# Kernel optimization log

Measured on AMD Instinct MI355X. Metric: run time of the kernel, lower is better.

The kernel has to match this reference:

```python
import jax, jax.numpy as jnp
import numpy as np

N = 100000   # nodes
E = 1600000  # edges
IN, HID, OUT = 128, 256, 64


def _glorot(key, shape):
    fan_in, fan_out = shape[1], shape[0]
    lim = (6.0 / (fan_in + fan_out)) ** 0.5
    return jax.random.uniform(key, shape, jnp.float32, -lim, lim)


def setup_inputs() -> dict:
    key = jax.random.key(0)
    ks = jax.random.split(key, 8)
    x = jax.random.normal(ks[0], (N, IN), jnp.float32)
    edge_index = jax.random.randint(ks[1], (2, E), 0, N, jnp.int64)
    # SAGEConv params: lin_l (neighbor path, has bias), lin_r (root path, no bias)
    return {
        "x": x,
        "edge_index": edge_index,
        "W1_l": _glorot(ks[2], (HID, IN)),
        "b1": jnp.zeros((HID,), jnp.float32),
        "W1_r": _glorot(ks[3], (HID, IN)),
        "W2_l": _glorot(ks[4], (OUT, HID)),
        "b2": jnp.zeros((OUT,), jnp.float32),
        "W2_r": _glorot(ks[5], (OUT, HID)),
    }


def _sage_conv(x, src, dst, W_l, b, W_r):
    # mean aggregation of neighbor features at destination nodes
    msg = x[src]                                             # [E, d] gather
    agg = jax.ops.segment_sum(msg, dst, num_segments=N)      # [N, d]
    cnt = jax.ops.segment_sum(jnp.ones((src.shape[0],), jnp.float32), dst,
                              num_segments=N)                # [N]
    mean = agg / jnp.maximum(cnt, 1.0)[:, None]
    return mean @ W_l.T + b + x @ W_r.T


def reference(x, edge_index, W1_l, b1, W1_r, W2_l, b2, W2_r):
    src, dst = edge_index[0], edge_index[1]
    h = jax.nn.relu(_sage_conv(x, src, dst, W1_l, b1, W1_r))
    # dropout is identity in eval mode
    return _sage_conv(h, src, dst, W2_l, b2, W2_r)
```

## Files before the change

kernel.cpp:

```cpp
#include <hip/hip_runtime.h>
#include <hip/hip_bf16.h>

#define NNODE 100000
#define NEDGE 1600000
#define NBBLK 512
#define CHUNK (NEDGE / NBBLK)
#define NB2 ((NNODE + 1023) >> 10)

typedef __attribute__((ext_vector_type(8))) short bf16x8;
typedef __attribute__((ext_vector_type(4))) float f32x4;
typedef __attribute__((ext_vector_type(2))) float f32x2;

__device__ __forceinline__ unsigned short f2bf(float f){
  unsigned u = __float_as_uint(f);
  u += 0x7fffu + ((u >> 16) & 1u);
  return (unsigned short)(u >> 16);
}
__device__ __forceinline__ unsigned pk2(float a, float b){
  return (unsigned)f2bf(a) | ((unsigned)f2bf(b) << 16);
}
__device__ __forceinline__ float bflo(unsigned v){ return __uint_as_float(v << 16); }
__device__ __forceinline__ float bfhi(unsigned v){ return __uint_as_float(v & 0xffff0000u); }

__global__ __launch_bounds__(256) void k_xh(const float* __restrict__ x,
                                            unsigned* __restrict__ A1u,
                                            unsigned* __restrict__ x8u,
                                            const int* __restrict__ dst,
                                            unsigned* __restrict__ gh){
  int bid = blockIdx.x;
  if (bid < NBBLK){
    __shared__ unsigned h[NB2];
    for (int t = threadIdx.x; t < NB2; t += 256) h[t] = 0;
    __syncthreads();
    int base = bid * CHUNK;
    for (int j = threadIdx.x; j < CHUNK; j += 256)
      atomicAdd(&h[dst[base + j] >> 10], 1u);
    __syncthreads();
    for (int t = threadIdx.x; t < NB2; t += 256) gh[bid * NB2 + t] = h[t];
    return;
  }
  int i = (bid - NBBLK) * 256 + threadIdx.x;
  if (i >= NNODE * 32) return;
  float4 v = ((const float4*)x)[i];
  int e = i * 4;
  int row = e >> 7, c = e & 127;
  unsigned* d = A1u + (size_t)row * 128 + 64 + (c >> 1);
  d[0] = pk2(v.x, v.y);
  d[1] = pk2(v.z, v.w);
  unsigned p = (unsigned)__builtin_amdgcn_cvt_pk_fp8_f32(v.x, v.y, 0, false);
  p = (unsigned)__builtin_amdgcn_cvt_pk_fp8_f32(v.z, v.w, (int)p, true);
  x8u[(size_t)row * 32 + (c >> 2)] = p;
}

__global__ __launch_bounds__(512) void k_scan512(const unsigned* __restrict__ gh,
                                                 unsigned* __restrict__ gbase,
                                                 unsigned* __restrict__ btot){
  int b = blockIdx.x, t = threadIdx.x;
  int lane = t & 63, wv = t >> 6;
  unsigned v = gh[t * NB2 + b];
  unsigned s = v;
  #pragma unroll
  for (int off = 1; off < 64; off <<= 1){
    unsigned u = __shfl_up(s, off, 64);
    if (lane >= off) s += u;
  }
  __shared__ unsigned wsum[8];
  if (lane == 63) wsum[wv] = s;
  __syncthreads();
  unsigned woff = 0;
  for (int w = 0; w < wv; ++w) woff += wsum[w];
  gbase[t * NB2 + b] = woff + s - v;
  if (t == 511) btot[b] = woff + s;
}

__global__ __launch_bounds__(128) void k_scanb(const unsigned* __restrict__ btot,
                                               unsigned* __restrict__ bbase,
                                               unsigned* __restrict__ rowptr){
  __shared__ unsigned buf[128];
  int tid = threadIdx.x;
  unsigned v = (tid < NB2) ? btot[tid] : 0u;
  buf[tid] = v;
  __syncthreads();
  #pragma unroll
  for (int off = 1; off < 128; off <<= 1){
    unsigned t = (tid >= off) ? buf[tid - off] : 0u;
    __syncthreads();
    buf[tid] += t;
    __syncthreads();
  }
  if (tid < NB2) bbase[tid] = buf[tid] - v;
  if (tid == 0){ bbase[NB2] = NEDGE; rowptr[NNODE] = NEDGE; }
}

__global__ __launch_bounds__(256) void k_binscat(const int* __restrict__ src,
                                                 const int* __restrict__ dst,
                                                 const unsigned* __restrict__ gbase,
                                                 const unsigned* __restrict__ bbase,
                                                 unsigned* __restrict__ pairs){
  __shared__ unsigned cur[NB2];
  for (int t = threadIdx.x; t < NB2; t += 256)
    cur[t] = bbase[t] + gbase[blockIdx.x * NB2 + t];
  __syncthreads();
  int base = blockIdx.x * CHUNK;
  for (int j = threadIdx.x; j < CHUNK; j += 256){
    int s = src[base + j], d = dst[base + j];
    unsigned p = atomicAdd(&cur[d >> 10], 1u);
    pairs[p] = ((unsigned)s << 10) | (unsigned)(d & 1023);
  }
}

__global__ __launch_bounds__(1024) void k_buildcsr(const unsigned* __restrict__ bbase,
                                                   const unsigned* __restrict__ pairs,
                                                   unsigned* __restrict__ rowptr,
                                                   unsigned* __restrict__ col){
  __shared__ unsigned hist[1024];
  __shared__ unsigned wsum[16];
  const int b = blockIdx.x, tid = threadIdx.x;
  const int lane = tid & 63, wv = tid >> 6;
  const unsigned e0 = bbase[b], e1 = bbase[b + 1];
  const int nb0 = b << 10;
  hist[tid] = 0;
  __syncthreads();
  for (unsigned j = e0 + tid; j < e1; j += 1024)
    atomicAdd(&hist[pairs[j] & 1023u], 1u);
  __syncthreads();
  unsigned v = hist[tid];
  unsigned s = v;
  #pragma unroll
  for (int off = 1; off < 64; off <<= 1){
    unsigned u = __shfl_up(s, off, 64);
    if (lane >= off) s += u;
  }
  if (lane == 63) wsum[wv] = s;
  __syncthreads();
  unsigned woff = 0;
  for (int w = 0; w < wv; ++w) woff += wsum[w];
  unsigned gpos = e0 + woff + s - v;
  if (nb0 + tid < NNODE) rowptr[nb0 + tid] = gpos;
  __syncthreads();
  hist[tid] = gpos;
  __syncthreads();
  for (unsigned j = e0 + tid; j < e1; j += 1024){
    unsigned e = pairs[j];
    unsigned p = atomicAdd(&hist[e & 1023u], 1u);
    col[p] = e >> 10;
  }
}

__global__ void k_wcvt(const float* __restrict__ W1l, const float* __restrict__ W1r,
                       const float* __restrict__ W2l, const float* __restrict__ W2r,
                       unsigned short* __restrict__ Bwt1, unsigned short* __restrict__ Bwt2){
  int i = blockIdx.x * 256 + threadIdx.x;
  if (i < 256 * 256){
    int n = i >> 8, k = i & 255;
    float v = (k < 128) ? W1l[n * 128 + k] : W1r[n * 128 + (k - 128)];
    Bwt1[i] = f2bf(v);
  }
  int i2 = i - 256 * 256;
  if (i2 >= 0 && i2 < 128 * 256){
    int n = i2 >> 8, k = i2 & 255;
    float v = (n < 64) ? W2l[n * 256 + k] : W2r[(n - 64) * 256 + k];
    Bwt2[i2] = f2bf(v);
  }
}

__global__ __launch_bounds__(256) void k_agg1(const unsigned* __restrict__ rowptr,
                                              const unsigned* __restrict__ col,
                                              const unsigned* __restrict__ x8u,
                                              unsigned* __restrict__ A1u){
  int gw = (blockIdx.x * 256 + threadIdx.x) >> 6;
  int lane = threadIdx.x & 63;
  if (gw >= NNODE) return;
  unsigned s0 = rowptr[gw], s1 = rowptr[gw + 1];
  const int sel = lane >> 4, u = lane & 15;
  const uint2* x82 = (const uint2*)x8u;
  float a0=0.f,a1=0.f,a2=0.f,a3=0.f,a4=0.f,a5=0.f,a6=0.f,a7=0.f;
  f32x2 p;
  unsigned j = s0;
  for (; j + 15 < s1; j += 16){
    unsigned ca = col[j + sel], cb = col[j + 4 + sel];
    unsigned cc = col[j + 8 + sel], cd = col[j + 12 + sel];
    uint2 va = x82[(size_t)ca * 16 + u];
    uint2 vb = x82[(size_t)cb * 16 + u];
    uint2 vc = x82[(size_t)cc * 16 + u];
    uint2 vd = x82[(size_t)cd * 16 + u];
    p = __builtin_amdgcn_cvt_pk_f32_fp8((int)va.x, false); a0+=p.x; a1+=p.y;
    p = __builtin_amdgcn_cvt_pk_f32_fp8((int)va.x, true ); a2+=p.x; a3+=p.y;
    p = __builtin_amdgcn_cvt_pk_f32_fp8((int)va.y, false); a4+=p.x; a5+=p.y;
    p = __builtin_amdgcn_cvt_pk_f32_fp8((int)va.y, true ); a6+=p.x; a7+=p.y;
    p = __builtin_amdgcn_cvt_pk_f32_fp8((int)vb.x, false); a0+=p.x; a1+=p.y;
    p = __builtin_amdgcn_cvt_pk_f32_fp8((int)vb.x, true ); a2+=p.x; a3+=p.y;
    p = __builtin_amdgcn_cvt_pk_f32_fp8((int)vb.y, false); a4+=p.x; a5+=p.y;
    p = __builtin_amdgcn_cvt_pk_f32_fp8((int)vb.y, true ); a6+=p.x; a7+=p.y;
    p = __builtin_amdgcn_cvt_pk_f32_fp8((int)vc.x, false); a0+=p.x; a1+=p.y;
    p = __builtin_amdgcn_cvt_pk_f32_fp8((int)vc.x, true ); a2+=p.x; a3+=p.y;
    p = __builtin_amdgcn_cvt_pk_f32_fp8((int)vc.y, false); a4+=p.x; a5+=p.y;
    p = __builtin_amdgcn_cvt_pk_f32_fp8((int)vc.y, true ); a6+=p.x; a7+=p.y;
    p = __builtin_amdgcn_cvt_pk_f32_fp8((int)vd.x, false); a0+=p.x; a1+=p.y;
    p = __builtin_amdgcn_cvt_pk_f32_fp8((int)vd.x, true ); a2+=p.x; a3+=p.y;
    p = __builtin_amdgcn_cvt_pk_f32_fp8((int)vd.y, false); a4+=p.x; a5+=p.y;
    p = __builtin_amdgcn_cvt_pk_f32_fp8((int)vd.y, true ); a6+=p.x; a7+=p.y;
  }
  for (; j + 3 < s1; j += 4){
    unsigned ca = col[j + sel];
    uint2 va = x82[(size_t)ca * 16 + u];
    p = __builtin_amdgcn_cvt_pk_f32_fp8((int)va.x, false); a0+=p.x; a1+=p.y;
    p = __builtin_amdgcn_cvt_pk_f32_fp8((int)va.x, true ); a2+=p.x; a3+=p.y;
    p = __builtin_amdgcn_cvt_pk_f32_fp8((int)va.y, false); a4+=p.x; a5+=p.y;
    p = __builtin_amdgcn_cvt_pk_f32_fp8((int)va.y, true ); a6+=p.x; a7+=p.y;
  }
  int rem = (int)(s1 - j);
  if (sel < rem){
    unsigned ca = col[j + sel];
    uint2 va = x82[(size_t)ca * 16 + u];
    p = __builtin_amdgcn_cvt_pk_f32_fp8((int)va.x, false); a0+=p.x; a1+=p.y;
    p = __builtin_amdgcn_cvt_pk_f32_fp8((int)va.x, true ); a2+=p.x; a3+=p.y;
    p = __builtin_amdgcn_cvt_pk_f32_fp8((int)va.y, false); a4+=p.x; a5+=p.y;
    p = __builtin_amdgcn_cvt_pk_f32_fp8((int)va.y, true ); a6+=p.x; a7+=p.y;
  }
  a0 += __shfl_xor(a0, 16, 64); a1 += __shfl_xor(a1, 16, 64);
  a2 += __shfl_xor(a2, 16, 64); a3 += __shfl_xor(a3, 16, 64);
  a4 += __shfl_xor(a4, 16, 64); a5 += __shfl_xor(a5, 16, 64);
  a6 += __shfl_xor(a6, 16, 64); a7 += __shfl_xor(a7, 16, 64);
  a0 += __shfl_xor(a0, 32, 64); a1 += __shfl_xor(a1, 32, 64);
  a2 += __shfl_xor(a2, 32, 64); a3 += __shfl_xor(a3, 32, 64);
  a4 += __shfl_xor(a4, 32, 64); a5 += __shfl_xor(a5, 32, 64);
  a6 += __shfl_xor(a6, 32, 64); a7 += __shfl_xor(a7, 32, 64);
  if (lane < 16){
    float inv = 1.f / fmaxf((float)(s1 - s0), 1.f);
    uint4 w;
    w.x = pk2(a0 * inv, a1 * inv);
    w.y = pk2(a2 * inv, a3 * inv);
    w.z = pk2(a4 * inv, a5 * inv);
    w.w = pk2(a6 * inv, a7 * inv);
    *(uint4*)(A1u + (size_t)gw * 128 + 4 * lane) = w;
  }
}

template<int BN, bool RELU, bool BIAS, int MODE>
__global__ __launch_bounds__(256) void k_gemm(const unsigned short* __restrict__ A,
                                              const unsigned short* __restrict__ B,
                                              const float* __restrict__ bias,
                                              unsigned short* __restrict__ C,
                                              unsigned char* __restrict__ z8,
                                              unsigned short* __restrict__ r16,
                                              int nrows){
  constexpr int NF = BN / 64;
  __shared__ unsigned short a_t[64 * 64];
  __shared__ unsigned short b_t[BN * 64];
  const int tid = threadIdx.x, wave = tid >> 6, lane = tid & 63;
  const int row0 = blockIdx.x * 64;
  char* ab = (char*)a_t;
  char* bb = (char*)b_t;

  f32x4 acc[4][NF];
  #pragma unroll
  for (int m = 0; m < 4; ++m)
    #pragma unroll
    for (int n = 0; n < NF; ++n)
      acc[m][n] = (f32x4){0.f, 0.f, 0.f, 0.f};

  for (int kt = 0; kt < 4; ++kt){
    {
      int r = tid >> 2;
      int gr = row0 + r; if (gr > nrows - 1) gr = nrows - 1;
      const uint4* s4 = (const uint4*)(A + (size_t)gr * 256 + kt * 64);
      int c0 = (tid & 3) * 2;
      uint4 v0 = s4[c0], v1 = s4[c0 + 1];
      *(uint4*)(ab + r * 128 + ((c0 * 16) ^ ((r & 7) << 4))) = v0;
      *(uint4*)(ab + r * 128 + (((c0 + 1) * 16) ^ ((r & 7) << 4))) = v1;
    }
    {
      constexpr int CPT = BN / 32;
      #pragma unroll
      for (int c = 0; c < CPT; ++c){
        int gc = tid * CPT + c;
        int n = gc >> 3, ck = gc & 7;
        uint4 v = ((const uint4*)(B + (size_t)n * 256 + kt * 64))[ck];
        *(uint4*)(bb + n * 128 + ((ck * 16) ^ ((n & 7) << 4))) = v;
      }
    }
    __syncthreads();
    #pragma unroll
    for (int kk = 0; kk < 2; ++kk){
      int k2 = (kk * 32 + ((lane >> 4) * 8)) * 2;
      bf16x8 af[4];
      #pragma unroll
      for (int m = 0; m < 4; ++m){
        int rr = m * 16 + (lane & 15);
        af[m] = *(const bf16x8*)(ab + rr * 128 + (k2 ^ ((rr & 7) << 4)));
      }
      #pragma unroll
      for (int n = 0; n < NF; ++n){
        int cc = wave * (16 * NF) + n * 16 + (lane & 15);
        bf16x8 bfv = *(const bf16x8*)(bb + cc * 128 + (k2 ^ ((cc & 7) << 4)));
        #pragma unroll
        for (int m = 0; m < 4; ++m)
          acc[m][n] = __builtin_amdgcn_mfma_f32_16x16x32_bf16(af[m], bfv, acc[m][n], 0, 0, 0);
      }
    }
    __syncthreads();
  }
  #pragma unroll
  for (int m = 0; m < 4; ++m){
    int rbase = row0 + m * 16 + ((lane >> 4) << 2);
    #pragma unroll
    for (int r = 0; r < 4; ++r){
      if (rbase + r < nrows){
        #pragma unroll
        for (int n = 0; n < NF; ++n){
          int cc = wave * (16 * NF) + n * 16 + (lane & 15);
          float v = acc[m][n][r];
          if (BIAS) v += bias[cc];
          if (RELU) v = fmaxf(v, 0.f);
          if (MODE == 0){
            C[(size_t)(rbase + r) * BN + cc] = f2bf(v);
          } else {
            if (cc < 64)
              z8[(size_t)(rbase + r) * 64 + cc] =
                (unsigned char)__builtin_amdgcn_cvt_pk_fp8_f32(v, v, 0, false);
            else
              r16[(size_t)(rbase + r) * 64 + (cc - 64)] = f2bf(v);
          }
        }
      }
    }
  }
}

__global__ __launch_bounds__(256) void k_agg2(const unsigned* __restrict__ rowptr,
                                              const unsigned* __restrict__ col,
                                              const unsigned* __restrict__ z8u,
                                              const unsigned* __restrict__ r16u,
                                              const float* __restrict__ b2,
                                              float* __restrict__ out){
  int gw = (blockIdx.x * 256 + threadIdx.x) >> 6;
  int lane = threadIdx.x & 63;
  if (gw >= NNODE) return;
  unsigned s0 = rowptr[gw], s1 = rowptr[gw + 1];
  const int sel = lane >> 4, u = lane & 15;
  float a0=0.f,a1=0.f,a2=0.f,a3=0.f;
  f32x2 p;
  unsigned j = s0;
  for (; j + 15 < s1; j += 16){
    unsigned ca = col[j + sel], cb = col[j + 4 + sel];
    unsigned cc = col[j + 8 + sel], cd = col[j + 12 + sel];
    unsigned va = z8u[(size_t)ca * 16 + u];
    unsigned vb = z8u[(size_t)cb * 16 + u];
    unsigned vc = z8u[(size_t)cc * 16 + u];
    unsigned vd = z8u[(size_t)cd * 16 + u];
    p = __builtin_amdgcn_cvt_pk_f32_fp8((int)va, false); a0+=p.x; a1+=p.y;
    p = __builtin_amdgcn_cvt_pk_f32_fp8((int)va, true ); a2+=p.x; a3+=p.y;
    p = __builtin_amdgcn_cvt_pk_f32_fp8((int)vb, false); a0+=p.x; a1+=p.y;
    p = __builtin_amdgcn_cvt_pk_f32_fp8((int)vb, true ); a2+=p.x; a3+=p.y;
    p = __builtin_amdgcn_cvt_pk_f32_fp8((int)vc, false); a0+=p.x; a1+=p.y;
    p = __builtin_amdgcn_cvt_pk_f32_fp8((int)vc, true ); a2+=p.x; a3+=p.y;
    p = __builtin_amdgcn_cvt_pk_f32_fp8((int)vd, false); a0+=p.x; a1+=p.y;
    p = __builtin_amdgcn_cvt_pk_f32_fp8((int)vd, true ); a2+=p.x; a3+=p.y;
  }
  for (; j + 3 < s1; j += 4){
    unsigned ca = col[j + sel];
    unsigned va = z8u[(size_t)ca * 16 + u];
    p = __builtin_amdgcn_cvt_pk_f32_fp8((int)va, false); a0+=p.x; a1+=p.y;
    p = __builtin_amdgcn_cvt_pk_f32_fp8((int)va, true ); a2+=p.x; a3+=p.y;
  }
  int rem = (int)(s1 - j);
  if (sel < rem){
    unsigned ca = col[j + sel];
    unsigned va = z8u[(size_t)ca * 16 + u];
    p = __builtin_amdgcn_cvt_pk_f32_fp8((int)va, false); a0+=p.x; a1+=p.y;
    p = __builtin_amdgcn_cvt_pk_f32_fp8((int)va, true ); a2+=p.x; a3+=p.y;
  }
  a0 += __shfl_xor(a0, 16, 64); a1 += __shfl_xor(a1, 16, 64);
  a2 += __shfl_xor(a2, 16, 64); a3 += __shfl_xor(a3, 16, 64);
  a0 += __shfl_xor(a0, 32, 64); a1 += __shfl_xor(a1, 32, 64);
  a2 += __shfl_xor(a2, 32, 64); a3 += __shfl_xor(a3, 32, 64);
  if (lane < 16){
    float inv = 1.f / fmaxf((float)(s1 - s0), 1.f);
    uint2 rv = ((const uint2*)(r16u + (size_t)gw * 32))[lane];
    float4 bv = ((const float4*)b2)[lane];
    float4 res;
    res.x = a0 * inv + bflo(rv.x) + bv.x;
    res.y = a1 * inv + bfhi(rv.x) + bv.y;
    res.z = a2 * inv + bflo(rv.y) + bv.z;
    res.w = a3 * inv + bfhi(rv.y) + bv.w;
    ((float4*)out)[(size_t)gw * 16 + lane] = res;
  }
}

extern "C" void kernel_launch(void* const* d_in, const int* in_sizes, int n_in,
                              void* d_out, int out_size, void* d_ws, size_t ws_size,
                              hipStream_t stream) {
  const float* x   = (const float*)d_in[0];
  const int*   ei  = (const int*)d_in[1];
  const float* W1l = (const float*)d_in[2];
  const float* b1  = (const float*)d_in[3];
  const float* W1r = (const float*)d_in[4];
  const float* W2l = (const float*)d_in[5];
  const float* b2  = (const float*)d_in[6];
  const float* W2r = (const float*)d_in[7];
  float* out = (float*)d_out;

  char* ws = (char*)d_ws;
  size_t off = 0;
  auto alloc = [&](size_t bytes) -> void* {
    void* p = ws + off;
    off = (off + bytes + 255) & ~(size_t)255;
    return p;
  };
  unsigned* rowptr = (unsigned*)alloc((size_t)(NNODE + 1) * 4);
  unsigned* col    = (unsigned*)alloc((size_t)NEDGE * 4);
  unsigned* pairs  = (unsigned*)alloc((size_t)NEDGE * 4);
  unsigned* gh     = (unsigned*)alloc((size_t)NBBLK * NB2 * 4);
  unsigned* gbase  = (unsigned*)alloc((size_t)NBBLK * NB2 * 4);
  unsigned* btot   = (unsigned*)alloc((size_t)NB2 * 4);
  unsigned* bbase  = (unsigned*)alloc((size_t)(NB2 + 1) * 4);
  unsigned short* A1   = (unsigned short*)alloc((size_t)NNODE * 256 * 2);
  unsigned short* h    = (unsigned short*)alloc((size_t)NNODE * 256 * 2);
  unsigned short* r16  = (unsigned short*)alloc((size_t)NNODE * 64 * 2);
  unsigned* x8u        = (unsigned*)alloc((size_t)NNODE * 32 * 4);
  unsigned char* z8    = (unsigned char*)alloc((size_t)NNODE * 64);
  unsigned short* Bwt1 = (unsigned short*)alloc(256 * 256 * 2);
  unsigned short* Bwt2 = (unsigned short*)alloc(128 * 256 * 2);

  const int* srcv = ei;
  const int* dstv = ei + NEDGE;

  k_xh<<<NBBLK + (NNODE * 32 + 255) / 256, 256, 0, stream>>>(x, (unsigned*)A1, x8u, dstv, gh);
  k_scan512<<<NB2, 512, 0, stream>>>(gh, gbase, btot);
  k_scanb<<<1, 128, 0, stream>>>(btot, bbase, rowptr);
  k_binscat<<<NBBLK, 256, 0, stream>>>(srcv, dstv, gbase, bbase, pairs);
  k_buildcsr<<<NB2, 1024, 0, stream>>>(bbase, pairs, rowptr, col);

  k_wcvt<<<(256 * 256 + 128 * 256 + 255) / 256, 256, 0, stream>>>(W1l, W1r, W2l, W2r, Bwt1, Bwt2);

  k_agg1<<<(NNODE + 3) / 4, 256, 0, stream>>>(rowptr, col, x8u, (unsigned*)A1);

  int gblocks = (NNODE + 63) / 64;
  k_gemm<256, true,  true,  0><<<gblocks, 256, 0, stream>>>(A1, Bwt1, b1, h, nullptr, nullptr, NNODE);
  k_gemm<128, false, false, 2><<<gblocks, 256, 0, stream>>>(h,  Bwt2, nullptr, nullptr, z8, r16, NNODE);

  k_agg2<<<(NNODE + 3) / 4, 256, 0, stream>>>(rowptr, col, (const unsigned*)z8, (const unsigned*)r16, b2, out);
}
```

Before: 314.2 us.

## Fold scans and weight conversion into fewer kernels; use finer buckets and 128-row GEMM tiles

The CSR build now uses 512-node buckets instead of 1024-node buckets, which gives 196 buckets. The separate bucket-base scan kernel is removed, and each binscat and buildcsr block recomputes that scan redundantly in shared memory. The weight bf16 conversion is merged into the first x-conversion/histogram kernel, so two launches are dropped. The GEMM kernels move to 512-thread blocks covering 128 rows, with waves split 2x4 so each staged B tile is reused across more rows. The cost is redundant scan work in every block and more shared memory per GEMM block, which may lower occupancy.

```diff
diff --git a/kernel.cpp b/kernel.cpp
--- a/kernel.cpp
+++ b/kernel.cpp
@@ -5,7 +5,9 @@
 #define NEDGE 1600000
 #define NBBLK 512
 #define CHUNK (NEDGE / NBBLK)
-#define NB2 ((NNODE + 1023) >> 10)
+#define NBUCK ((NNODE + 511) >> 9)
+#define XB ((NNODE * 32 + 255) / 256)
+#define WB 384
 
 typedef __attribute__((ext_vector_type(8))) short bf16x8;
 typedef __attribute__((ext_vector_type(4))) float f32x4;
@@ -26,30 +28,50 @@
                                             unsigned* __restrict__ A1u,
                                             unsigned* __restrict__ x8u,
                                             const int* __restrict__ dst,
-                                            unsigned* __restrict__ gh){
+                                            unsigned* __restrict__ gh,
+                                            const float* __restrict__ W1l,
+                                            const float* __restrict__ W1r,
+                                            const float* __restrict__ W2l,
+                                            const float* __restrict__ W2r,
+                                            unsigned short* __restrict__ Bwt1,
+                                            unsigned short* __restrict__ Bwt2){
   int bid = blockIdx.x;
   if (bid < NBBLK){
-    __shared__ unsigned h[NB2];
-    for (int t = threadIdx.x; t < NB2; t += 256) h[t] = 0;
+    __shared__ unsigned h[NBUCK];
+    for (int t = threadIdx.x; t < NBUCK; t += 256) h[t] = 0;
     __syncthreads();
     int base = bid * CHUNK;
     for (int j = threadIdx.x; j < CHUNK; j += 256)
-      atomicAdd(&h[dst[base + j] >> 10], 1u);
-    __syncthreads();
-    for (int t = threadIdx.x; t < NB2; t += 256) gh[bid * NB2 + t] = h[t];
+      atomicAdd(&h[dst[base + j] >> 9], 1u);
+    __syncthreads();
+    for (int t = threadIdx.x; t < NBUCK; t += 256) gh[bid * NBUCK + t] = h[t];
     return;
   }
-  int i = (bid - NBBLK) * 256 + threadIdx.x;
-  if (i >= NNODE * 32) return;
-  float4 v = ((const float4*)x)[i];
-  int e = i * 4;
-  int row = e >> 7, c = e & 127;
-  unsigned* d = A1u + (size_t)row * 128 + 64 + (c >> 1);
-  d[0] = pk2(v.x, v.y);
-  d[1] = pk2(v.z, v.w);
-  unsigned p = (unsigned)__builtin_amdgcn_cvt_pk_fp8_f32(v.x, v.y, 0, false);
-  p = (unsigned)__builtin_amdgcn_cvt_pk_fp8_f32(v.z, v.w, (int)p, true);
-  x8u[(size_t)row * 32 + (c >> 2)] = p;
+  if (bid < NBBLK + XB){
+    int i = (bid - NBBLK) * 256 + threadIdx.x;
+    if (i >= NNODE * 32) return;
+    float4 v = ((const float4*)x)[i];
+    int e = i * 4;
+    int row = e >> 7, c = e & 127;
+    unsigned* d = A1u + (size_t)row * 128 + 64 + (c >> 1);
+    d[0] = pk2(v.x, v.y);
+    d[1] = pk2(v.z, v.w);
+    unsigned p = (unsigned)__builtin_amdgcn_cvt_pk_fp8_f32(v.x, v.y, 0, false);
+    p = (unsigned)__builtin_amdgcn_cvt_pk_fp8_f32(v.z, v.w, (int)p, true);
+    x8u[(size_t)row * 32 + (c >> 2)] = p;
+    return;
+  }
+  int i = (bid - NBBLK - XB) * 256 + threadIdx.x;
+  if (i < 256 * 256){
+    int n = i >> 8, k = i & 255;
+    float v = (k < 128) ? W1l[n * 128 + k] : W1r[n * 128 + (k - 128)];
+    Bwt1[i] = f2bf(v);
+  } else if (i < 256 * 256 + 128 * 256){
+    int i2 = i - 256 * 256;
+    int n = i2 >> 8, k = i2 & 255;
+    float v = (n < 64) ? W2l[n * 256 + k] : W2r[(n - 64) * 256 + k];
+    Bwt2[i2] = f2bf(v);
+  }
 }
 
 __global__ __launch_bounds__(512) void k_scan512(const unsigned* __restrict__ gh,
@@ -57,7 +79,7 @@
                                                  unsigned* __restrict__ btot){
   int b = blockIdx.x, t = threadIdx.x;
   int lane = t & 63, wv = t >> 6;
-  unsigned v = gh[t * NB2 + b];
+  unsigned v = gh[t * NBUCK + b];
   unsigned s = v;
   #pragma unroll
   for (int off = 1; off < 64; off <<= 1){
@@ -69,60 +91,72 @@
   __syncthreads();
   unsigned woff = 0;
   for (int w = 0; w < wv; ++w) woff += wsum[w];
-  gbase[t * NB2 + b] = woff + s - v;
+  gbase[t * NBUCK + b] = woff + s - v;
   if (t == 511) btot[b] = woff + s;
-}
-
-__global__ __launch_bounds__(128) void k_scanb(const unsigned* __restrict__ btot,
-                                               unsigned* __restrict__ bbase,
-                                               unsigned* __restrict__ rowptr){
-  __shared__ unsigned buf[128];
-  int tid = threadIdx.x;
-  unsigned v = (tid < NB2) ? btot[tid] : 0u;
-  buf[tid] = v;
-  __syncthreads();
-  #pragma unroll
-  for (int off = 1; off < 128; off <<= 1){
-    unsigned t = (tid >= off) ? buf[tid - off] : 0u;
-    __syncthreads();
-    buf[tid] += t;
-    __syncthreads();
-  }
-  if (tid < NB2) bbase[tid] = buf[tid] - v;
-  if (tid == 0){ bbase[NB2] = NEDGE; rowptr[NNODE] = NEDGE; }
 }
 
 __global__ __launch_bounds__(256) void k_binscat(const int* __restrict__ src,
                                                  const int* __restrict__ dst,
                                                  const unsigned* __restrict__ gbase,
-                                                 const unsigned* __restrict__ bbase,
+                                                 const unsigned* __restrict__ btot,
                                                  unsigned* __restrict__ pairs){
-  __shared__ unsigned cur[NB2];
-  for (int t = threadIdx.x; t < NB2; t += 256)
-    cur[t] = bbase[t] + gbase[blockIdx.x * NB2 + t];
+  __shared__ unsigned sb[256];
+  __shared__ unsigned cur[NBUCK];
+  int t = threadIdx.x;
+  unsigned v = (t < NBUCK) ? btot[t] : 0u;
+  sb[t] = v;
+  __syncthreads();
+  #pragma unroll
+  for (int off = 1; off < 256; off <<= 1){
+    unsigned u = (t >= off) ? sb[t - off] : 0u;
+    __syncthreads();
+    sb[t] += u;
+    __syncthreads();
+  }
+  if (t < NBUCK) cur[t] = (sb[t] - v) + gbase[blockIdx.x * NBUCK + t];
   __syncthreads();
   int base = blockIdx.x * CHUNK;
-  for (int j = threadIdx.x; j < CHUNK; j += 256){
+  for (int j = t; j < CHUNK; j += 256){
     int s = src[base + j], d = dst[base + j];
-    unsigned p = atomicAdd(&cur[d >> 10], 1u);
-    pairs[p] = ((unsigned)s << 10) | (unsigned)(d & 1023);
-  }
-}
-
-__global__ __launch_bounds__(1024) void k_buildcsr(const unsigned* __restrict__ bbase,
-                                                   const unsigned* __restrict__ pairs,
-                                                   unsigned* __restrict__ rowptr,
-                                                   unsigned* __restrict__ col){
-  __shared__ unsigned hist[1024];
-  __shared__ unsigned wsum[16];
+    unsigned p = atomicAdd(&cur[d >> 9], 1u);
+    pairs[p] = ((unsigned)s << 9) | (unsigned)(d & 511);
+  }
+}
+
+__global__ __launch_bounds__(512) void k_buildcsr(const unsigned* __restrict__ btot,
+                                                  const unsigned* __restrict__ pairs,
+                                                  unsigned* __restrict__ rowptr,
+                                                  unsigned* __restrict__ col){
+  __shared__ unsigned sb[256];
+  __shared__ unsigned hist[512];
+  __shared__ unsigned wsum[8];
+  __shared__ unsigned se0, se1;
   const int b = blockIdx.x, tid = threadIdx.x;
   const int lane = tid & 63, wv = tid >> 6;
-  const unsigned e0 = bbase[b], e1 = bbase[b + 1];
-  const int nb0 = b << 10;
+  if (tid < 256){
+    unsigned v = (tid < NBUCK) ? btot[tid] : 0u;
+    sb[tid] = v;
+  }
+  __syncthreads();
+  #pragma unroll
+  for (int off = 1; off < 256; off <<= 1){
+    unsigned u = 0;
+    if (tid < 256 && tid >= off) u = sb[tid - off];
+    __syncthreads();
+    if (tid < 256) sb[tid] += u;
+    __syncthreads();
+  }
+  if (tid == 0){
+    se1 = sb[b];
+    se0 = sb[b] - btot[b];
+    if (b == 0) rowptr[NNODE] = NEDGE;
+  }
   hist[tid] = 0;
   __syncthreads();
-  for (unsigned j = e0 + tid; j < e1; j += 1024)
-    atomicAdd(&hist[pairs[j] & 1023u], 1u);
+  const unsigned e0 = se0, e1 = se1;
+  const int nb0 = b << 9;
+  for (unsigned j = e0 + tid; j < e1; j += 512)
+    atomicAdd(&hist[pairs[j] & 511u], 1u);
   __syncthreads();
   unsigned v = hist[tid];
   unsigned s = v;
@@ -140,27 +174,10 @@
   __syncthreads();
   hist[tid] = gpos;
   __syncthreads();
-  for (unsigned j = e0 + tid; j < e1; j += 1024){
+  for (unsigned j = e0 + tid; j < e1; j += 512){
     unsigned e = pairs[j];
-    unsigned p = atomicAdd(&hist[e & 1023u], 1u);
-    col[p] = e >> 10;
-  }
-}
-
-__global__ void k_wcvt(const float* __restrict__ W1l, const float* __restrict__ W1r,
-                       const float* __restrict__ W2l, const float* __restrict__ W2r,
-                       unsigned short* __restrict__ Bwt1, unsigned short* __restrict__ Bwt2){
-  int i = blockIdx.x * 256 + threadIdx.x;
-  if (i < 256 * 256){
-    int n = i >> 8, k = i & 255;
-    float v = (k < 128) ? W1l[n * 128 + k] : W1r[n * 128 + (k - 128)];
-    Bwt1[i] = f2bf(v);
-  }
-  int i2 = i - 256 * 256;
-  if (i2 >= 0 && i2 < 128 * 256){
-    int n = i2 >> 8, k = i2 & 255;
-    float v = (n < 64) ? W2l[n * 256 + k] : W2r[(n - 64) * 256 + k];
-    Bwt2[i2] = f2bf(v);
+    unsigned p = atomicAdd(&hist[e & 511u], 1u);
+    col[p] = e >> 9;
   }
 }
 
@@ -238,7 +255,7 @@
 }
 
 template<int BN, bool RELU, bool BIAS, int MODE>
-__global__ __launch_bounds__(256) void k_gemm(const unsigned short* __restrict__ A,
+__global__ __launch_bounds__(512) void k_gemm(const unsigned short* __restrict__ A,
                                               const unsigned short* __restrict__ B,
                                               const float* __restrict__ bias,
                                               unsigned short* __restrict__ C,
@@ -246,10 +263,11 @@
                                               unsigned short* __restrict__ r16,
                                               int nrows){
   constexpr int NF = BN / 64;
-  __shared__ unsigned short a_t[64 * 64];
+  __shared__ unsigned short a_t[128 * 64];
   __shared__ unsigned short b_t[BN * 64];
   const int tid = threadIdx.x, wave = tid >> 6, lane = tid & 63;
-  const int row0 = blockIdx.x * 64;
+  const int wr = wave >> 2, wc = wave & 3;
+  const int row0 = blockIdx.x * 128;
   char* ab = (char*)a_t;
   char* bb = (char*)b_t;
 
@@ -271,7 +289,7 @@
       *(uint4*)(ab + r * 128 + (((c0 + 1) * 16) ^ ((r & 7) << 4))) = v1;
     }
     {
-      constexpr int CPT = BN / 32;
+      constexpr int CPT = BN / 64;
       #pragma unroll
       for (int c = 0; c < CPT; ++c){
         int gc = tid * CPT + c;
@@ -287,12 +305,12 @@
       bf16x8 af[4];
       #pragma unroll
       for (int m = 0; m < 4; ++m){
-        int rr = m * 16 + (lane & 15);
+        int rr = wr * 64 + m * 16 + (lane & 15);
         af[m] = *(const bf16x8*)(ab + rr * 128 + (k2 ^ ((rr & 7) << 4)));
       }
       #pragma unroll
       for (int n = 0; n < NF; ++n){
-        int cc = wave * (16 * NF) + n * 16 + (lane & 15);
+        int cc = wc * (16 * NF) + n * 16 + (lane & 15);
         bf16x8 bfv = *(const bf16x8*)(bb + cc * 128 + (k2 ^ ((cc & 7) << 4)));
         #pragma unroll
         for (int m = 0; m < 4; ++m)
@@ -303,13 +321,13 @@
   }
   #pragma unroll
   for (int m = 0; m < 4; ++m){
-    int rbase = row0 + m * 16 + ((lane >> 4) << 2);
+    int rbase = row0 + wr * 64 + m * 16 + ((lane >> 4) << 2);
     #pragma unroll
     for (int r = 0; r < 4; ++r){
       if (rbase + r < nrows){
         #pragma unroll
         for (int n = 0; n < NF; ++n){
-          int cc = wave * (16 * NF) + n * 16 + (lane & 15);
+          int cc = wc * (16 * NF) + n * 16 + (lane & 15);
           float v = acc[m][n][r];
           if (BIAS) v += bias[cc];
           if (RELU) v = fmaxf(v, 0.f);
@@ -411,10 +429,9 @@
   unsigned* rowptr = (unsigned*)alloc((size_t)(NNODE + 1) * 4);
   unsigned* col    = (unsigned*)alloc((size_t)NEDGE * 4);
   unsigned* pairs  = (unsigned*)alloc((size_t)NEDGE * 4);
-  unsigned* gh     = (unsigned*)alloc((size_t)NBBLK * NB2 * 4);
-  unsigned* gbase  = (unsigned*)alloc((size_t)NBBLK * NB2 * 4);
-  unsigned* btot   = (unsigned*)alloc((size_t)NB2 * 4);
-  unsigned* bbase  = (unsigned*)alloc((size_t)(NB2 + 1) * 4);
+  unsigned* gh     = (unsigned*)alloc((size_t)NBBLK * NBUCK * 4);
+  unsigned* gbase  = (unsigned*)alloc((size_t)NBBLK * NBUCK * 4);
+  unsigned* btot   = (unsigned*)alloc((size_t)NBUCK * 4);
   unsigned short* A1   = (unsigned short*)alloc((size_t)NNODE * 256 * 2);
   unsigned short* h    = (unsigned short*)alloc((size_t)NNODE * 256 * 2);
   unsigned short* r16  = (unsigned short*)alloc((size_t)NNODE * 64 * 2);
@@ -426,19 +443,17 @@
   const int* srcv = ei;
   const int* dstv = ei + NEDGE;
 
-  k_xh<<<NBBLK + (NNODE * 32 + 255) / 256, 256, 0, stream>>>(x, (unsigned*)A1, x8u, dstv, gh);
-  k_scan512<<<NB2, 512, 0, stream>>>(gh, gbase, btot);
-  k_scanb<<<1, 128, 0, stream>>>(btot, bbase, rowptr);
-  k_binscat<<<NBBLK, 256, 0, stream>>>(srcv, dstv, gbase, bbase, pairs);
-  k_buildcsr<<<NB2, 1024, 0, stream>>>(bbase, pairs, rowptr, col);
-
-  k_wcvt<<<(256 * 256 + 128 * 256 + 255) / 256, 256, 0, stream>>>(W1l, W1r, W2l, W2r, Bwt1, Bwt2);
+  k_xh<<<NBBLK + XB + WB, 256, 0, stream>>>(x, (unsigned*)A1, x8u, dstv, gh,
+                                            W1l, W1r, W2l, W2r, Bwt1, Bwt2);
+  k_scan512<<<NBUCK, 512, 0, stream>>>(gh, gbase, btot);
+  k_binscat<<<NBBLK, 256, 0, stream>>>(srcv, dstv, gbase, btot, pairs);
+  k_buildcsr<<<NBUCK, 512, 0, stream>>>(btot, pairs, rowptr, col);
 
   k_agg1<<<(NNODE + 3) / 4, 256, 0, stream>>>(rowptr, col, x8u, (unsigned*)A1);
 
-  int gblocks = (NNODE + 63) / 64;
-  k_gemm<256, true,  true,  0><<<gblocks, 256, 0, stream>>>(A1, Bwt1, b1, h, nullptr, nullptr, NNODE);
-  k_gemm<128, false, false, 2><<<gblocks, 256, 0, stream>>>(h,  Bwt2, nullptr, nullptr, z8, r16, NNODE);
+  int gblocks = (NNODE + 127) / 128;
+  k_gemm<256, true,  true,  0><<<gblocks, 512, 0, stream>>>(A1, Bwt1, b1, h, nullptr, nullptr, NNODE);
+  k_gemm<128, false, false, 2><<<gblocks, 512, 0, stream>>>(h,  Bwt2, nullptr, nullptr, z8, r16, NNODE);
 
   k_agg2<<<(NNODE + 3) / 4, 256, 0, stream>>>(rowptr, col, (const unsigned*)z8, (const unsigned*)r16, b2, out);
 }
```

After: 297.2 us. -5.4%, faster.
